# Optimization experiments

Hardware: AMD Instinct MI355X
Metric: run time of the kernel (lower is better)

The kernel has to match this reference:

```python
import jax, jax.numpy as jnp
import numpy as np
import math

Z, H, G, S = 4, 16, 4, 4096          # batch, q heads, kv groups, seq len
BLOCK = 32                            # compression block size
NB = S // BLOCK                       # number of compressed KV blocks (128)
DQK, DV = 128, 128                    # head dims


def setup_inputs() -> dict:
    key = jax.random.key(0)
    k1, k2, k3 = jax.random.split(key, 3)
    q = jax.random.normal(k1, (Z, H, S, DQK), jnp.float32)
    k_blocks = jax.random.normal(k2, (Z, G, NB, DQK), jnp.float32)
    v_blocks = jax.random.normal(k3, (Z, G, NB, DV), jnp.float32)
    # block j covers tokens [j*BLOCK, (j+1)*BLOCK), so it 'ends' at position (j+1)*BLOCK-1
    block_ends = (jnp.arange(1, NB + 1) * BLOCK - 1).astype(jnp.int32)
    return {"q": q, "k_blocks": k_blocks, "v_blocks": v_blocks, "block_ends": block_ends}


def reference(q, k_blocks, v_blocks, block_ends):
    """NSA compression attention fwd: block-end causal masking over compressed KV blocks.
    q: [Z,H,S,Dqk]; k_blocks/v_blocks: [Z,G,NB,D]; block_ends: [NB] int.
    Query at position m attends to compressed block j iff block_ends[j] <= m.
    Rows with no valid block output zeros (matching the kernel's l_i==0 path)."""
    Zb, Hb, Sb, Dq = q.shape
    Gb = k_blocks.shape[1]
    sm_scale = 1.0 / math.sqrt(Dq)
    # GQA: head h -> kv group h // (H // G)
    qg = (q * sm_scale).reshape(Zb, Gb, Hb // Gb, Sb, Dq)
    s = jnp.einsum('zghsd,zgnd->zghsn', qg, k_blocks)        # [Z,G,H/G,S,NB]
    pos = jnp.arange(Sb)
    mask = block_ends[None, :] <= pos[:, None]               # [S,NB]
    s_masked = jnp.where(mask, s, -jnp.inf)
    m = jnp.max(s_masked, axis=-1, keepdims=True)            # online-softmax max (M)
    m_safe = jnp.where(jnp.isfinite(m), m, 0.0)
    p = jnp.where(mask, jnp.exp(s_masked - jax.lax.stop_gradient(m_safe)), 0.0)
    l = jnp.sum(p, axis=-1, keepdims=True)                   # softmax denom (exp(L-M))
    o = jnp.einsum('zghsn,zgnv->zghsv', p, v_blocks)
    o = jnp.where(l > 0, o / jnp.where(l > 0, l, 1.0), 0.0)
    return o.reshape(Zb, Hb, Sb, -1)                         # [Z,H,S,Dv]
```

## Files before the change

kernel.cpp:

```cpp
#include <hip/hip_runtime.h>


#define Zc 4
#define Hc 16
#define Gc 4
#define Sc 4096
#define NBc 128
#define Dc 128
#define VST 136

typedef __attribute__((ext_vector_type(8))) short short8;
typedef __attribute__((ext_vector_type(4))) float float4v;

__device__ inline unsigned pk2bf(float a, float b) {
    union { float f; unsigned u; } x, y; x.f = a; y.f = b;
    return __builtin_amdgcn_perm(y.u + 0x8000u, x.u + 0x8000u, 0x07060302u);
}
__device__ inline short8 mkfrag(float4v f0, float4v f1) {
    union { short8 v; unsigned d[4]; } u;
    u.d[0] = pk2bf(f0[0], f0[1]);
    u.d[1] = pk2bf(f0[2], f0[3]);
    u.d[2] = pk2bf(f1[0], f1[1]);
    u.d[3] = pk2bf(f1[2], f1[3]);
    return u.v;
}

__device__ inline void do_gemm1(const short* __restrict__ Ksh, short8 (&qf)[4][2],
                                float4v (&acc)[8][2], int c_max, int l16, int quad) {
    #pragma unroll
    for (int c = 0; c < 8; c++)
        #pragma unroll
        for (int t = 0; t < 2; t++) acc[c][t] = (float4v)0.f;
    #pragma unroll
    for (int dk = 0; dk < 4; dk++)
        #pragma unroll
        for (int c = 0; c < 8; c++)
            if (c < c_max) {
                short8 a = *(const short8*)(Ksh + (c * 16 + l16) * VST + dk * 32 + quad * 8);
                acc[c][0] = __builtin_amdgcn_mfma_f32_16x16x32_bf16(a, qf[dk][0], acc[c][0], 0, 0, 0);
                acc[c][1] = __builtin_amdgcn_mfma_f32_16x16x32_bf16(a, qf[dk][1], acc[c][1], 0, 0, 0);
            }
}

__device__ inline void do_softmax(float4v (&acc)[8][2], unsigned (&Ppk)[8][2][2],
                                  int m0, int c_max, int l16, int quad) {
    #pragma unroll
    for (int c = 0; c < 8; c++)
        #pragma unroll
        for (int t = 0; t < 2; t++) { Ppk[c][t][0] = 0u; Ppk[c][t][1] = 0u; }
    #pragma unroll
    for (int t = 0; t < 2; t++) {
        const int mg = m0 + t * 16 + l16;
        int nv = (mg + 1) >> 5; if (nv > NBc) nv = NBc;
        float mx = -1e30f;
        #pragma unroll
        for (int c = 0; c < 8; c++)
            if (c < c_max)
                #pragma unroll
                for (int r = 0; r < 4; r++) {
                    const int j = c * 16 + quad * 4 + r;
                    float s = acc[c][t][r];
                    s = (j < nv) ? s : -1e30f;
                    acc[c][t][r] = s;
                    mx = fmaxf(mx, s);
                }
        mx = fmaxf(mx, __shfl_xor(mx, 16, 64));
        mx = fmaxf(mx, __shfl_xor(mx, 32, 64));
        float ls = 0.f;
        #pragma unroll
        for (int c = 0; c < 8; c++)
            if (c < c_max)
                #pragma unroll
                for (int r = 0; r < 4; r++) {
                    float s = acc[c][t][r];
                    float p = (s > -1e29f) ? __expf(s - mx) : 0.f;
                    acc[c][t][r] = p;
                    ls += p;
                }
        ls += __shfl_xor(ls, 16, 64);
        ls += __shfl_xor(ls, 32, 64);
        const float inv = (ls > 0.f) ? 1.f / ls : 0.f;
        #pragma unroll
        for (int c = 0; c < 8; c++)
            if (c < c_max) {
                Ppk[c][t][0] = pk2bf(acc[c][t][0] * inv, acc[c][t][1] * inv);
                Ppk[c][t][1] = pk2bf(acc[c][t][2] * inv, acc[c][t][3] * inv);
            }
    }
}

__device__ inline void do_gemm2_store(const short* __restrict__ Vt, unsigned (&Ppk)[8][2][2],
                                      float* __restrict__ obase, int kbi_max,
                                      int l16, int quad) {
    float4v oacc[8][2];
    #pragma unroll
    for (int c = 0; c < 8; c++)
        #pragma unroll
        for (int t = 0; t < 2; t++) oacc[c][t] = (float4v)0.f;

    const int s0 = (((2 * quad) & 3) << 4) | l16;
    const int s1 = (((2 * quad + 1) & 3) << 4) | l16;
    const bool hi = (quad >= 2);

    #pragma unroll
    for (int kbi = 0; kbi < 4; kbi++)
        if (kbi < kbi_max) {
            short8 ap[2];
            #pragma unroll
            for (int t = 0; t < 2; t++) {
                const int c1 = 2 * kbi;
                unsigned w0a = (unsigned)__shfl((int)Ppk[c1    ][t][0], s0, 64);
                unsigned w0b = (unsigned)__shfl((int)Ppk[c1 + 1][t][0], s0, 64);
                unsigned w1a = (unsigned)__shfl((int)Ppk[c1    ][t][1], s0, 64);
                unsigned w1b = (unsigned)__shfl((int)Ppk[c1 + 1][t][1], s0, 64);
                unsigned w2a = (unsigned)__shfl((int)Ppk[c1    ][t][0], s1, 64);
                unsigned w2b = (unsigned)__shfl((int)Ppk[c1 + 1][t][0], s1, 64);
                unsigned w3a = (unsigned)__shfl((int)Ppk[c1    ][t][1], s1, 64);
                unsigned w3b = (unsigned)__shfl((int)Ppk[c1 + 1][t][1], s1, 64);
                union { short8 v; unsigned d[4]; } u;
                u.d[0] = hi ? w0b : w0a;
                u.d[1] = hi ? w1b : w1a;
                u.d[2] = hi ? w2b : w2a;
                u.d[3] = hi ? w3b : w3a;
                ap[t] = u.v;
            }
            #pragma unroll
            for (int c = 0; c < 8; c++) {
                short8 bv = *(const short8*)(Vt + (c * 16 + l16) * VST + kbi * 32 + quad * 8);
                #pragma unroll
                for (int t = 0; t < 2; t++)
                    oacc[c][t] = __builtin_amdgcn_mfma_f32_16x16x32_bf16(ap[t], bv, oacc[c][t], 0, 0, 0);
            }
        }

    #pragma unroll
    for (int t = 0; t < 2; t++)
        #pragma unroll
        for (int rr = 0; rr < 4; rr++) {
            const int row = t * 16 + quad * 4 + rr;
            #pragma unroll
            for (int c = 0; c < 8; c++)
                obase[(size_t)row * Dc + c * 16 + l16] = oacc[c][t][rr];
        }
}

__global__ __launch_bounds__(256, 2)
void nsa_fwd(const float* __restrict__ q, const float* __restrict__ kb,
             const float* __restrict__ vb, float* __restrict__ out) {
    __shared__ __align__(16) short KV[NBc * VST];

    const int b    = blockIdx.x;
    const int h    = blockIdx.y, z = blockIdx.z, g = h >> 2;
    const int tid  = threadIdx.x;
    const int wq   = tid >> 6;
    const int lane = tid & 63;
    const int l16  = lane & 15;
    const int quad = lane >> 4;

    const int bx0 = b, bx1 = 31 - b;
    const int nv0 = 4 * bx0 + wq + 1;
    const int nv1 = 4 * bx1 + wq + 1;
    const int cmax0 = (nv0 + 15) >> 4, kbi0 = (nv0 + 31) >> 5;
    const int cmax1 = (nv1 + 15) >> 4, kbi1 = (nv1 + 31) >> 5;
    const int nv_hi  = 4 * bx1 + 4;
    const int cst    = (nv_hi + 15) >> 4;
    const int nstage = ((nv_hi + 31) >> 5) << 5;

    const int m0_0 = bx0 * 128 + wq * 32;
    const int m0_1 = bx1 * 128 + wq * 32;
    const float sm = 0.08838834764831845f;

    const float* qb0 = q + ((size_t)(z * Hc + h) * Sc + m0_0) * Dc;
    float4v q0raw[4][2][2];
    #pragma unroll
    for (int dk = 0; dk < 4; dk++)
        #pragma unroll
        for (int t = 0; t < 2; t++) {
            const float* s = qb0 + (size_t)(t * 16 + l16) * Dc + dk * 32 + quad * 8;
            q0raw[dk][t][0] = *(const float4v*)s;
            q0raw[dk][t][1] = *(const float4v*)(s + 4);
        }

    const float* ksrc = kb + (size_t)(z * Gc + g) * NBc * Dc;
    #pragma unroll
    for (int it = 0; it < 8; it++)
        if (it < cst) {
            int i = it * 256 + tid;
            int n = i >> 4, c8 = i & 15;
            const float* s = ksrc + (size_t)n * Dc + c8 * 8;
            float4v f0 = *(const float4v*)s, f1 = *(const float4v*)(s + 4);
            *(short8*)(KV + n * VST + c8 * 8) = mkfrag(f0, f1);
        }

    short8 qf[4][2];
    #pragma unroll
    for (int dk = 0; dk < 4; dk++)
        #pragma unroll
        for (int t = 0; t < 2; t++)
            qf[dk][t] = mkfrag(q0raw[dk][t][0] * sm, q0raw[dk][t][1] * sm);

    __syncthreads();

    const float* qb1 = q + ((size_t)(z * Hc + h) * Sc + m0_1) * Dc;
    float4v q1raw[4][2][2];
    #pragma unroll
    for (int dk = 0; dk < 4; dk++)
        #pragma unroll
        for (int t = 0; t < 2; t++) {
            const float* s = qb1 + (size_t)(t * 16 + l16) * Dc + dk * 32 + quad * 8;
            q1raw[dk][t][0] = *(const float4v*)s;
            q1raw[dk][t][1] = *(const float4v*)(s + 4);
        }

    float4v acc[8][2];
    unsigned Ppk0[8][2][2], Ppk1[8][2][2];

    do_gemm1(KV, qf, acc, cmax0, l16, quad);
    do_softmax(acc, Ppk0, m0_0, cmax0, l16, quad);

    #pragma unroll
    for (int dk = 0; dk < 4; dk++)
        #pragma unroll
        for (int t = 0; t < 2; t++)
            qf[dk][t] = mkfrag(q1raw[dk][t][0] * sm, q1raw[dk][t][1] * sm);

    const float* vsrc = vb + (size_t)(z * Gc + g) * NBc * Dc;
    const int n2 = lane * 2;
    const bool vact = (n2 < nstage);
    float4v vraw[8][2];
    #pragma unroll
    for (int it = 0; it < 8; it++) {
        const int c = it * 4 + wq;
        if (vact) {
            vraw[it][0] = *(const float4v*)(vsrc + (size_t)n2 * Dc + c * 4);
            vraw[it][1] = *(const float4v*)(vsrc + (size_t)(n2 + 1) * Dc + c * 4);
        }
    }

    do_gemm1(KV, qf, acc, cmax1, l16, quad);

    __syncthreads();

    #pragma unroll
    for (int it = 0; it < 8; it++) {
        const int c = it * 4 + wq;
        if (vact) {
            #pragma unroll
            for (int k2 = 0; k2 < 4; k2++)
                *(unsigned*)(KV + (c * 4 + k2) * VST + n2) = pk2bf(vraw[it][0][k2], vraw[it][1][k2]);
        }
    }
    do_softmax(acc, Ppk1, m0_1, cmax1, l16, quad);

    __syncthreads();

    float* ob0 = out + ((size_t)(z * Hc + h) * Sc + m0_0) * Dc;
    float* ob1 = out + ((size_t)(z * Hc + h) * Sc + m0_1) * Dc;
    do_gemm2_store(KV, Ppk0, ob0, kbi0, l16, quad);
    do_gemm2_store(KV, Ppk1, ob1, kbi1, l16, quad);
}

extern "C" void kernel_launch(void* const* d_in, const int* in_sizes, int n_in,
                              void* d_out, int out_size, void* d_ws, size_t ws_size,
                              hipStream_t stream) {
    const float* q  = (const float*)d_in[0];
    const float* kb = (const float*)d_in[1];
    const float* vb = (const float*)d_in[2];
    float* out = (float*)d_out;
    dim3 grid(16, Hc, Zc);
    nsa_fwd<<<grid, dim3(256), 0, stream>>>(q, kb, vb, out);
}
```

Before: 249.2 us.

## Use 512-thread blocks with separate K and V shared buffers staged upfront

Doubles the block to 512 threads, with two 256-thread subgroups each handling a mirrored pair of query tiles. This halves the grid and shares the K/V staging across twice as many queries. K and the transposed V now live in separate LDS arrays that are both filled at kernel start. That removes the mid-kernel barriers and the register-held V prefetch, and lets the first tile's output GEMM run before the second tile's QK. In exchange, LDS use per block doubles, staging is sized for the larger subgroup, and the launch bound of 4 blocks of 512 threads may squeeze registers and occupancy.

```diff
diff --git a/kernel.cpp b/kernel.cpp
--- a/kernel.cpp
+++ b/kernel.cpp
@@ -144,27 +144,30 @@
         }
 }
 
-__global__ __launch_bounds__(256, 2)
+__global__ __launch_bounds__(512, 4)
 void nsa_fwd(const float* __restrict__ q, const float* __restrict__ kb,
              const float* __restrict__ vb, float* __restrict__ out) {
-    __shared__ __align__(16) short KV[NBc * VST];
+    __shared__ __align__(16) short Ksh[NBc * VST];
+    __shared__ __align__(16) short Vt[Dc * VST];
 
     const int b    = blockIdx.x;
     const int h    = blockIdx.y, z = blockIdx.z, g = h >> 2;
     const int tid  = threadIdx.x;
-    const int wq   = tid >> 6;
+    const int sgrp = tid >> 8;
+    const int wq   = (tid >> 6) & 3;
     const int lane = tid & 63;
     const int l16  = lane & 15;
     const int quad = lane >> 4;
 
-    const int bx0 = b, bx1 = 31 - b;
+    const int j   = 2 * b + sgrp;
+    const int bx0 = j, bx1 = 31 - j;
     const int nv0 = 4 * bx0 + wq + 1;
     const int nv1 = 4 * bx1 + wq + 1;
     const int cmax0 = (nv0 + 15) >> 4, kbi0 = (nv0 + 31) >> 5;
     const int cmax1 = (nv1 + 15) >> 4, kbi1 = (nv1 + 31) >> 5;
-    const int nv_hi  = 4 * bx1 + 4;
-    const int cst    = (nv_hi + 15) >> 4;
-    const int nstage = ((nv_hi + 31) >> 5) << 5;
+    const int nv_hi  = 128 - 8 * b;
+    const int kst    = (nv_hi + 31) >> 5;
+    const int nstage = kst << 5;
 
     const int m0_0 = bx0 * 128 + wq * 32;
     const int m0_1 = bx1 * 128 + wq * 32;
@@ -183,14 +186,32 @@
 
     const float* ksrc = kb + (size_t)(z * Gc + g) * NBc * Dc;
     #pragma unroll
-    for (int it = 0; it < 8; it++)
-        if (it < cst) {
-            int i = it * 256 + tid;
+    for (int it = 0; it < 4; it++)
+        if (it < kst) {
+            int i = it * 512 + tid;
             int n = i >> 4, c8 = i & 15;
             const float* s = ksrc + (size_t)n * Dc + c8 * 8;
             float4v f0 = *(const float4v*)s, f1 = *(const float4v*)(s + 4);
-            *(short8*)(KV + n * VST + c8 * 8) = mkfrag(f0, f1);
-        }
+            *(short8*)(Ksh + n * VST + c8 * 8) = mkfrag(f0, f1);
+        }
+
+    {
+        const float* vsrc = vb + (size_t)(z * Gc + g) * NBc * Dc;
+        const int vw = tid >> 6;
+        const int n2 = lane * 2;
+        const bool vact = (n2 < nstage);
+        #pragma unroll
+        for (int it = 0; it < 4; it++) {
+            const int c = it * 8 + vw;
+            if (vact) {
+                float4v fa = *(const float4v*)(vsrc + (size_t)n2 * Dc + c * 4);
+                float4v fb = *(const float4v*)(vsrc + (size_t)(n2 + 1) * Dc + c * 4);
+                #pragma unroll
+                for (int k2 = 0; k2 < 4; k2++)
+                    *(unsigned*)(Vt + (c * 4 + k2) * VST + n2) = pk2bf(fa[k2], fb[k2]);
+            }
+        }
+    }
 
     short8 qf[4][2];
     #pragma unroll
@@ -213,10 +234,10 @@
         }
 
     float4v acc[8][2];
-    unsigned Ppk0[8][2][2], Ppk1[8][2][2];
-
-    do_gemm1(KV, qf, acc, cmax0, l16, quad);
-    do_softmax(acc, Ppk0, m0_0, cmax0, l16, quad);
+    unsigned Ppk[8][2][2];
+
+    do_gemm1(Ksh, qf, acc, cmax0, l16, quad);
+    do_softmax(acc, Ppk, m0_0, cmax0, l16, quad);
 
     #pragma unroll
     for (int dk = 0; dk < 4; dk++)
@@ -224,40 +245,13 @@
         for (int t = 0; t < 2; t++)
             qf[dk][t] = mkfrag(q1raw[dk][t][0] * sm, q1raw[dk][t][1] * sm);
 
-    const float* vsrc = vb + (size_t)(z * Gc + g) * NBc * Dc;
-    const int n2 = lane * 2;
-    const bool vact = (n2 < nstage);
-    float4v vraw[8][2];
-    #pragma unroll
-    for (int it = 0; it < 8; it++) {
-        const int c = it * 4 + wq;
-        if (vact) {
-            vraw[it][0] = *(const float4v*)(vsrc + (size_t)n2 * Dc + c * 4);
-            vraw[it][1] = *(const float4v*)(vsrc + (size_t)(n2 + 1) * Dc + c * 4);
-        }
-    }
-
-    do_gemm1(KV, qf, acc, cmax1, l16, quad);
-
-    __syncthreads();
-
-    #pragma unroll
-    for (int it = 0; it < 8; it++) {
-        const int c = it * 4 + wq;
-        if (vact) {
-            #pragma unroll
-            for (int k2 = 0; k2 < 4; k2++)
-                *(unsigned*)(KV + (c * 4 + k2) * VST + n2) = pk2bf(vraw[it][0][k2], vraw[it][1][k2]);
-        }
-    }
-    do_softmax(acc, Ppk1, m0_1, cmax1, l16, quad);
-
-    __syncthreads();
-
     float* ob0 = out + ((size_t)(z * Hc + h) * Sc + m0_0) * Dc;
+    do_gemm2_store(Vt, Ppk, ob0, kbi0, l16, quad);
+
+    do_gemm1(Ksh, qf, acc, cmax1, l16, quad);
+    do_softmax(acc, Ppk, m0_1, cmax1, l16, quad);
     float* ob1 = out + ((size_t)(z * Hc + h) * Sc + m0_1) * Dc;
-    do_gemm2_store(KV, Ppk0, ob0, kbi0, l16, quad);
-    do_gemm2_store(KV, Ppk1, ob1, kbi1, l16, quad);
+    do_gemm2_store(Vt, Ppk, ob1, kbi1, l16, quad);
 }
 
 extern "C" void kernel_launch(void* const* d_in, const int* in_sizes, int n_in,
@@ -267,6 +261,6 @@
     const float* kb = (const float*)d_in[1];
     const float* vb = (const float*)d_in[2];
     float* out = (float*)d_out;
-    dim3 grid(16, Hc, Zc);
-    nsa_fwd<<<grid, dim3(256), 0, stream>>>(q, kb, vb, out);
-}
+    dim3 grid(8, Hc, Zc);
+    nsa_fwd<<<grid, dim3(512), 0, stream>>>(q, kb, vb, out);
+}
```

Result: slower. 277.7 us (+11.4%).
